# Optimization experiments

Hardware: AMD Instinct MI355X
Metric: run time of the kernel (lower is better)

Reference implementation:

```python
import jax, jax.numpy as jnp
import numpy as np

N_TOKENS = 524288
N_FEATURES = 128
N_MODELS = 16
N_LAYERS = 2


def setup_inputs() -> dict:
    key = jax.random.key(0)
    kx, kw, kb = jax.random.split(key, 3)
    x = jax.random.normal(kx, (N_TOKENS, N_FEATURES), dtype=jnp.float32)
    # per-expert, per-layer Linear weights in torch layout [out, in]
    scale = 1.0 / np.sqrt(N_FEATURES)
    W = jax.random.normal(kw, (N_MODELS, N_LAYERS, N_FEATURES, N_FEATURES), dtype=jnp.float32) * scale
    b = jax.random.normal(kb, (N_MODELS, N_LAYERS, N_FEATURES), dtype=jnp.float32) * scale
    return {"x": x, "W": W, "b": b}


def reference(x, W, b):
    # x: [N, F]; W: [M, L, F_out, F_in]; b: [M, L, F_out]
    # slices = M equal contiguous partitions of the token dim; each slice runs
    # through its own Linear+ReLU stack and is scattered back (here: reshape).
    M, L, Fo, Fi = W.shape
    xs = x.reshape(M, -1, Fi)  # [M, N/M, F] gathered slices
    for l in range(L):  # small fixed depth loop
        xs = jax.nn.relu(jnp.einsum('mnf,mgf->mng', xs, W[:, l]) + b[:, l][:, None, :])
    return xs.reshape(x.shape[0], Fo)
```

## Files before the change

### kernel.cpp

```cpp
#include <hip/hip_runtime.h>


#define NF   128
#define NM   16
#define NTOK 524288
#define TPM  (NTOK / NM)
#define BM   128
#define BPM  (TPM / BM)
#define WPAD 136

typedef __attribute__((ext_vector_type(8))) short bf16x8;
typedef __attribute__((ext_vector_type(4))) short bf16x4v;
typedef __attribute__((ext_vector_type(4))) float f32x4;
typedef unsigned int u32;

__device__ __forceinline__ unsigned short f2bf(float f) {
    union { float f; unsigned u; } v; v.f = f;
    unsigned r = v.u + 0x7FFFu + ((v.u >> 16) & 1u);
    return (unsigned short)(r >> 16);
}

__device__ alignas(16) unsigned short g_Wf[NM * 2 * NF * NF];

__global__ __launch_bounds__(256) void convw_kernel(const float* __restrict__ W) {
    const int idx  = blockIdx.x * 256 + threadIdx.x;
    const int lane = idx & 63;
    const int fid  = (idx >> 6) & 31;
    const int ml   = idx >> 11;
    const int row  = (fid >> 2) * 16 + (lane & 15);
    const int col  = (fid & 3) * 32 + (lane >> 4) * 8;
    const float* s = W + ((size_t)ml * NF + row) * NF + col;
    float4 a = *(const float4*)s;
    float4 c = *(const float4*)(s + 4);
    unsigned short* d = &g_Wf[(size_t)idx * 8];
    d[0] = f2bf(a.x); d[1] = f2bf(a.y); d[2] = f2bf(a.z); d[3] = f2bf(a.w);
    d[4] = f2bf(c.x); d[5] = f2bf(c.y); d[6] = f2bf(c.z); d[7] = f2bf(c.w);
}

__device__ __forceinline__ void load_lds16(const unsigned short* g, unsigned short* l) {
    __builtin_amdgcn_global_load_lds(
        (const __attribute__((address_space(1))) u32*)g,
        (__attribute__((address_space(3))) u32*)l, 16, 0, 0);
}

__global__ __launch_bounds__(512, 4) void mlp16_kernel(
        const float* __restrict__ x, const float* __restrict__ b,
        float* __restrict__ out) {
    __shared__ alignas(16) unsigned short buf0[BM * WPAD];
    __shared__ alignas(16) unsigned short sW1[NF * NF];
    __shared__ alignas(16) float sB[2 * NF];

    const int t    = threadIdx.x;
    const int w    = t >> 6;
    const int lane = t & 63;
    const int ln   = lane & 15;
    const int q    = lane >> 4;

    const int m    = blockIdx.x >> 8;
    const int tile = blockIdx.x & (BPM - 1);
    const int row0 = m * TPM + tile * BM;

    if (t < 2 * NF) sB[t] = b[m * 2 * NF + t];

    const unsigned short* wsrc = g_Wf + (size_t)m * 2 * NF * NF;
    #pragma unroll
    for (int i = 0; i < 4; ++i) {
        const int fid = w * 4 + i;
        load_lds16(wsrc + (size_t)(fid * 64 + lane) * 8, &buf0[fid * 512]);
        load_lds16(wsrc + NF * NF + (size_t)(fid * 64 + lane) * 8, &sW1[fid * 512]);
    }

    const float* xrow = x + (size_t)(row0 + w * 16 + ln) * NF;
    float4 xa[8];
    #pragma unroll
    for (int kt = 0; kt < 4; ++kt) {
        xa[2 * kt]     = *(const float4*)(xrow + kt * 32 + q * 8);
        xa[2 * kt + 1] = *(const float4*)(xrow + kt * 32 + q * 8 + 4);
    }

    __syncthreads();

    f32x4 acc[8];
    #pragma unroll
    for (int gt = 0; gt < 8; ++gt) acc[gt] = (f32x4){0.f, 0.f, 0.f, 0.f};

    #pragma unroll
    for (int kt = 0; kt < 4; ++kt) {
        const float4 a0 = xa[2 * kt], a1 = xa[2 * kt + 1];
        bf16x8 xb;
        xb[0] = (short)f2bf(a0.x); xb[1] = (short)f2bf(a0.y);
        xb[2] = (short)f2bf(a0.z); xb[3] = (short)f2bf(a0.w);
        xb[4] = (short)f2bf(a1.x); xb[5] = (short)f2bf(a1.y);
        xb[6] = (short)f2bf(a1.z); xb[7] = (short)f2bf(a1.w);
        #pragma unroll
        for (int gt = 0; gt < 8; ++gt) {
            bf16x8 wf = *(const bf16x8*)&buf0[((gt * 4 + kt) * 64 + lane) * 8];
            acc[gt] = __builtin_amdgcn_mfma_f32_16x16x32_bf16(wf, xb, acc[gt], 0, 0, 0);
        }
    }

    __syncthreads();

    #pragma unroll
    for (int gt = 0; gt < 8; ++gt) {
        const f32x4 bv = *(const f32x4*)&sB[gt * 16 + q * 4];
        bf16x4v yv;
        #pragma unroll
        for (int r = 0; r < 4; ++r) {
            float v = acc[gt][r] + bv[r];
            v = v > 0.f ? v : 0.f;
            yv[r] = (short)f2bf(v);
        }
        *(bf16x4v*)&buf0[(w * 16 + ln) * WPAD + gt * 16 + q * 4] = yv;
    }

    __syncthreads();

    f32x4 acc2[8];
    #pragma unroll
    for (int gt = 0; gt < 8; ++gt) acc2[gt] = (f32x4){0.f, 0.f, 0.f, 0.f};

    const unsigned short* yrow = &buf0[(w * 16 + ln) * WPAD];
    #pragma unroll
    for (int kt = 0; kt < 4; ++kt) {
        const bf16x8 yb = *(const bf16x8*)(yrow + kt * 32 + q * 8);
        #pragma unroll
        for (int gt = 0; gt < 8; ++gt) {
            bf16x8 wf = *(const bf16x8*)&sW1[((gt * 4 + kt) * 64 + lane) * 8];
            acc2[gt] = __builtin_amdgcn_mfma_f32_16x16x32_bf16(wf, yb, acc2[gt], 0, 0, 0);
        }
    }

    float* orow = out + (size_t)(row0 + w * 16 + ln) * NF;
    #pragma unroll
    for (int gt = 0; gt < 8; ++gt) {
        const f32x4 bv = *(const f32x4*)&sB[NF + gt * 16 + q * 4];
        float4 o;
        float v0 = acc2[gt][0] + bv[0]; o.x = v0 > 0.f ? v0 : 0.f;
        float v1 = acc2[gt][1] + bv[1]; o.y = v1 > 0.f ? v1 : 0.f;
        float v2 = acc2[gt][2] + bv[2]; o.z = v2 > 0.f ? v2 : 0.f;
        float v3 = acc2[gt][3] + bv[3]; o.w = v3 > 0.f ? v3 : 0.f;
        *(float4*)(orow + gt * 16 + q * 4) = o;
    }
}

extern "C" void kernel_launch(void* const* d_in, const int* in_sizes, int n_in,
                              void* d_out, int out_size, void* d_ws, size_t ws_size,
                              hipStream_t stream) {
    const float* x = (const float*)d_in[0];
    const float* W = (const float*)d_in[1];
    const float* b = (const float*)d_in[2];
    float* out = (float*)d_out;
    convw_kernel<<<dim3(256), dim3(256), 0, stream>>>(W);
    mlp16_kernel<<<dim3(NTOK / BM), dim3(512), 0, stream>>>(x, b, out);
}
```

Measured before the change: 441.8 us.

## Make blocks process multiple token tiles, reusing LDS weights and prefetching x

```diff
diff --git a/kernel.cpp b/kernel.cpp
--- a/kernel.cpp
+++ b/kernel.cpp
@@ -1,13 +1,14 @@
 #include <hip/hip_runtime.h>
 
 
-#define NF   128
-#define NM   16
-#define NTOK 524288
-#define TPM  (NTOK / NM)
-#define BM   128
-#define BPM  (TPM / BM)
-#define WPAD 136
+#define NF    128
+#define NM    16
+#define NTOK  524288
+#define TPM   (NTOK / NM)
+#define BM    128
+#define TILES 8
+#define BLKPM ((TPM / BM) / TILES)
+#define WPAD  136
 
 typedef __attribute__((ext_vector_type(8))) short bf16x8;
 typedef __attribute__((ext_vector_type(4))) short bf16x4v;
@@ -43,11 +44,12 @@
         (__attribute__((address_space(3))) u32*)l, 16, 0, 0);
 }
 
-__global__ __launch_bounds__(512, 4) void mlp16_kernel(
+__global__ __launch_bounds__(512, 2) void mlp16_kernel(
         const float* __restrict__ x, const float* __restrict__ b,
         float* __restrict__ out) {
-    __shared__ alignas(16) unsigned short buf0[BM * WPAD];
+    __shared__ alignas(16) unsigned short sW0[NF * NF];
     __shared__ alignas(16) unsigned short sW1[NF * NF];
+    __shared__ alignas(16) unsigned short sY[BM * WPAD];
     __shared__ alignas(16) float sB[2 * NF];
 
     const int t    = threadIdx.x;
@@ -56,9 +58,8 @@
     const int ln   = lane & 15;
     const int q    = lane >> 4;
 
-    const int m    = blockIdx.x >> 8;
-    const int tile = blockIdx.x & (BPM - 1);
-    const int row0 = m * TPM + tile * BM;
+    const int m  = blockIdx.x / BLKPM;
+    const int tg = blockIdx.x % BLKPM;
 
     if (t < 2 * NF) sB[t] = b[m * 2 * NF + t];
 
@@ -66,11 +67,16 @@
     #pragma unroll
     for (int i = 0; i < 4; ++i) {
         const int fid = w * 4 + i;
-        load_lds16(wsrc + (size_t)(fid * 64 + lane) * 8, &buf0[fid * 512]);
+        load_lds16(wsrc + (size_t)(fid * 64 + lane) * 8, &sW0[fid * 512]);
         load_lds16(wsrc + NF * NF + (size_t)(fid * 64 + lane) * 8, &sW1[fid * 512]);
     }
 
-    const float* xrow = x + (size_t)(row0 + w * 16 + ln) * NF;
+    const size_t tok0 = (size_t)m * TPM + (size_t)tg * (TILES * BM);
+    const float* xrow = x + (tok0 + (size_t)(w * 16 + ln)) * NF;
+    float*       orow = out + (tok0 + (size_t)(w * 16 + ln)) * NF;
+    unsigned short*       syw = &sY[(w * 16 + ln) * WPAD];
+    const unsigned short* syr = syw;
+
     float4 xa[8];
     #pragma unroll
     for (int kt = 0; kt < 4; ++kt) {
@@ -80,67 +86,77 @@
 
     __syncthreads();
 
-    f32x4 acc[8];
-    #pragma unroll
-    for (int gt = 0; gt < 8; ++gt) acc[gt] = (f32x4){0.f, 0.f, 0.f, 0.f};
+    for (int i = 0; i < TILES; ++i) {
+        bf16x8 xb[4];
+        #pragma unroll
+        for (int kt = 0; kt < 4; ++kt) {
+            const float4 a0 = xa[2 * kt], a1 = xa[2 * kt + 1];
+            bf16x8 v;
+            v[0] = (short)f2bf(a0.x); v[1] = (short)f2bf(a0.y);
+            v[2] = (short)f2bf(a0.z); v[3] = (short)f2bf(a0.w);
+            v[4] = (short)f2bf(a1.x); v[5] = (short)f2bf(a1.y);
+            v[6] = (short)f2bf(a1.z); v[7] = (short)f2bf(a1.w);
+            xb[kt] = v;
+        }
 
-    #pragma unroll
-    for (int kt = 0; kt < 4; ++kt) {
-        const float4 a0 = xa[2 * kt], a1 = xa[2 * kt + 1];
-        bf16x8 xb;
-        xb[0] = (short)f2bf(a0.x); xb[1] = (short)f2bf(a0.y);
-        xb[2] = (short)f2bf(a0.z); xb[3] = (short)f2bf(a0.w);
-        xb[4] = (short)f2bf(a1.x); xb[5] = (short)f2bf(a1.y);
-        xb[6] = (short)f2bf(a1.z); xb[7] = (short)f2bf(a1.w);
+        if (i + 1 < TILES) {
+            const float* p = xrow + (size_t)(i + 1) * (BM * NF);
+            #pragma unroll
+            for (int kt = 0; kt < 4; ++kt) {
+                xa[2 * kt]     = *(const float4*)(p + kt * 32 + q * 8);
+                xa[2 * kt + 1] = *(const float4*)(p + kt * 32 + q * 8 + 4);
+            }
+        }
+
+        f32x4 acc[8];
+        #pragma unroll
+        for (int gt = 0; gt < 8; ++gt) acc[gt] = *(const f32x4*)&sB[gt * 16 + q * 4];
+        #pragma unroll
+        for (int kt = 0; kt < 4; ++kt) {
+            #pragma unroll
+            for (int gt = 0; gt < 8; ++gt) {
+                bf16x8 wf = *(const bf16x8*)&sW0[((gt * 4 + kt) * 64 + lane) * 8];
+                acc[gt] = __builtin_amdgcn_mfma_f32_16x16x32_bf16(wf, xb[kt], acc[gt], 0, 0, 0);
+            }
+        }
+
         #pragma unroll
         for (int gt = 0; gt < 8; ++gt) {
-            bf16x8 wf = *(const bf16x8*)&buf0[((gt * 4 + kt) * 64 + lane) * 8];
-            acc[gt] = __builtin_amdgcn_mfma_f32_16x16x32_bf16(wf, xb, acc[gt], 0, 0, 0);
+            bf16x4v yv;
+            #pragma unroll
+            for (int r = 0; r < 4; ++r) {
+                float vv = acc[gt][r];
+                vv = vv > 0.f ? vv : 0.f;
+                yv[r] = (short)f2bf(vv);
+            }
+            *(bf16x4v*)&syw[gt * 16 + q * 4] = yv;
         }
-    }
+        asm volatile("" ::: "memory");
 
-    __syncthreads();
+        f32x4 acc2[8];
+        #pragma unroll
+        for (int gt = 0; gt < 8; ++gt) acc2[gt] = *(const f32x4*)&sB[NF + gt * 16 + q * 4];
+        #pragma unroll
+        for (int kt = 0; kt < 4; ++kt) {
+            const bf16x8 yb = *(const bf16x8*)(syr + kt * 32 + q * 8);
+            #pragma unroll
+            for (int gt = 0; gt < 8; ++gt) {
+                bf16x8 wf = *(const bf16x8*)&sW1[((gt * 4 + kt) * 64 + lane) * 8];
+                acc2[gt] = __builtin_amdgcn_mfma_f32_16x16x32_bf16(wf, yb, acc2[gt], 0, 0, 0);
+            }
+        }
+        asm volatile("" ::: "memory");
 
-    #pragma unroll
-    for (int gt = 0; gt < 8; ++gt) {
-        const f32x4 bv = *(const f32x4*)&sB[gt * 16 + q * 4];
-        bf16x4v yv;
-        #pragma unroll
-        for (int r = 0; r < 4; ++r) {
-            float v = acc[gt][r] + bv[r];
-            v = v > 0.f ? v : 0.f;
-            yv[r] = (short)f2bf(v);
-        }
-        *(bf16x4v*)&buf0[(w * 16 + ln) * WPAD + gt * 16 + q * 4] = yv;
-    }
-
-    __syncthreads();
-
-    f32x4 acc2[8];
-    #pragma unroll
-    for (int gt = 0; gt < 8; ++gt) acc2[gt] = (f32x4){0.f, 0.f, 0.f, 0.f};
-
-    const unsigned short* yrow = &buf0[(w * 16 + ln) * WPAD];
-    #pragma unroll
-    for (int kt = 0; kt < 4; ++kt) {
-        const bf16x8 yb = *(const bf16x8*)(yrow + kt * 32 + q * 8);
+        float* op = orow + (size_t)i * (BM * NF);
         #pragma unroll
         for (int gt = 0; gt < 8; ++gt) {
-            bf16x8 wf = *(const bf16x8*)&sW1[((gt * 4 + kt) * 64 + lane) * 8];
-            acc2[gt] = __builtin_amdgcn_mfma_f32_16x16x32_bf16(wf, yb, acc2[gt], 0, 0, 0);
+            float4 o;
+            float v0 = acc2[gt][0]; o.x = v0 > 0.f ? v0 : 0.f;
+            float v1 = acc2[gt][1]; o.y = v1 > 0.f ? v1 : 0.f;
+            float v2 = acc2[gt][2]; o.z = v2 > 0.f ? v2 : 0.f;
+            float v3 = acc2[gt][3]; o.w = v3 > 0.f ? v3 : 0.f;
+            *(float4*)(op + gt * 16 + q * 4) = o;
         }
-    }
-
-    float* orow = out + (size_t)(row0 + w * 16 + ln) * NF;
-    #pragma unroll
-    for (int gt = 0; gt < 8; ++gt) {
-        const f32x4 bv = *(const f32x4*)&sB[NF + gt * 16 + q * 4];
-        float4 o;
-        float v0 = acc2[gt][0] + bv[0]; o.x = v0 > 0.f ? v0 : 0.f;
-        float v1 = acc2[gt][1] + bv[1]; o.y = v1 > 0.f ? v1 : 0.f;
-        float v2 = acc2[gt][2] + bv[2]; o.z = v2 > 0.f ? v2 : 0.f;
-        float v3 = acc2[gt][3] + bv[3]; o.w = v3 > 0.f ? v3 : 0.f;
-        *(float4*)(orow + gt * 16 + q * 4) = o;
     }
 }
 
@@ -152,5 +168,5 @@
     const float* b = (const float*)d_in[2];
     float* out = (float*)d_out;
     convw_kernel<<<dim3(256), dim3(256), 0, stream>>>(W);
-    mlp16_kernel<<<dim3(NTOK / BM), dim3(512), 0, stream>>>(x, b, out);
+    mlp16_kernel<<<dim3(NM * BLKPM), dim3(512), 0, stream>>>(x, b, out);
 }
```

Measured after the change: 448.7 us. About the same (+1.5%).
